# Optimization experiments

Hardware: AMD Instinct MI355X
Metric: run time of the kernel (lower is better)

The kernel has to match this reference:

```python
import jax, jax.numpy as jnp
import numpy as np

D = 256      # n_feature
LVL = 17     # tree depth (leaf levels)
MIX = 20     # M mixture components


def _lstm_cell(x, h, c, Wih, Whh, bih, bhh):
    # torch.nn.LSTMCell gate order: i, f, g, o
    g = x @ Wih.T + bih + h @ Whh.T + bhh
    i, f, gg, o = jnp.split(g, 4, axis=1)
    c2 = jax.nn.sigmoid(f) * c + jax.nn.sigmoid(i) * jnp.tanh(gg)
    return jax.nn.sigmoid(o) * jnp.tanh(c2), c2


def _get_parameter(y, M):
    parts = jnp.split(y[:, :13 * M], 13, axis=1)
    pi = jax.nn.softmax(parts[0], axis=1)
    mu_x, mu_y = parts[1], parts[2]
    sx, sy = jnp.exp(parts[3]), jnp.exp(parts[4])
    rho_xy = jnp.tanh(parts[5])
    mu_a, mu_b = parts[6], parts[7]
    sa, sb = jnp.exp(parts[8]), jnp.exp(parts[9])
    rho_ab = jnp.tanh(parts[10])
    mu_s, ss = parts[11], jnp.exp(parts[12])
    q = jax.nn.softmax(y[:, -3:], axis=1)
    return (pi, mu_x, mu_y, sx, sy, rho_xy, mu_a, mu_b, sa, sb, rho_ab, mu_s, ss, q)


def _bvn_logpdf(dx, dy, mx, my, sx, sy, rho):
    zx = (dx - mx) / sx
    zy = (dy - my) / sy
    Z = zx ** 2 + zy ** 2 - 2.0 * rho * zx * zy
    return -Z / (2.0 * (1.0 - rho ** 2)) - jnp.log(2.0 * jnp.pi * sx * sy * jnp.sqrt(1.0 - rho ** 2))


def _nll(pt, prm):
    # pt: [n, 8] = (x, y, a, b, slope, p1, p2, p3); prm: GMM parameters, each [n, M]
    pi, mx, my, sx, sy, rxy, ma, mb, sa, sb, rab, ms, ss, q = prm
    lpi = jnp.log(pi)
    dx, dy, da, db, ds = (pt[:, k:k + 1] for k in range(5))
    p = pt[:, 5:8]
    lse = jax.scipy.special.logsumexp
    lxy = lse(lpi + _bvn_logpdf(dx, dy, mx, my, sx, sy, rxy), axis=1)
    lab = lse(lpi + _bvn_logpdf(da, db, ma, mb, sa, sb, rab), axis=1)
    lsl = lse(lpi - (ds - ms) ** 2 / (2.0 * ss ** 2) - jnp.log(jnp.sqrt(2.0 * jnp.pi) * ss), axis=1)
    pen = -(p * jnp.log(q)).sum(axis=1)
    return -(lxy + lab + lsl) + pen


def _expected_pos(prm):
    pi, mx, my, sx, sy, rxy, ma, mb, sa, sb, rab, ms, ss, q = prm
    e = lambda m: (pi * m).sum(axis=1)
    return jnp.concatenate([jnp.stack([e(mx), e(my), e(ma), e(mb), e(ms)], axis=1), q], axis=1)


def _levels(I_flat):
    # I_flat is bottom-up concatenation of per-level [ni,3] blocks of a full binary tree
    n_int = I_flat.shape[0]
    L = int(np.log2(n_int + 1))
    sizes = [2 ** (L - 1 - i) for i in range(L)]
    offs = np.concatenate([[0], np.cumsum(sizes)])
    return [I_flat[offs[i]:offs[i + 1]] for i in range(L)]


def setup_inputs() -> dict:
    key = jax.random.key(0)
    ks = jax.random.split(key, 16)
    N = 2 ** (LVL + 1) - 1  # 262143 total nodes
    # heap-layout full binary tree: children of i are 2i+1, 2i+2; bottom-up levels
    blocks = []
    for l in range(LVL - 1, -1, -1):
        f = np.arange(2 ** l - 1, 2 ** (l + 1) - 1)
        blocks.append(np.stack([2 * f + 1, 2 * f + 2, f], axis=1))
    I_flat = jnp.asarray(np.concatenate(blocks, 0), dtype=jnp.int32)
    s = 0.05
    return {
        "X": jax.random.normal(ks[0], (N, 8), jnp.float32),
        "Feature": jax.random.normal(ks[1], (N, D), jnp.float32),
        "I_flat": I_flat,
        "W_ih_e": jax.random.normal(ks[2], (4 * (D // 2), 8), jnp.float32) * s,
        "W_hh_e": jax.random.normal(ks[3], (4 * (D // 2), D // 2), jnp.float32) * s,
        "b_ih_e": jax.random.normal(ks[4], (4 * (D // 2),), jnp.float32) * s,
        "b_hh_e": jax.random.normal(ks[5], (4 * (D // 2),), jnp.float32) * s,
        "fc_h_W": jax.random.normal(ks[6], (2 * D, D), jnp.float32) * s,
        "fc_h_b": jax.random.normal(ks[7], (2 * D,), jnp.float32) * s,
        "W_ih_d": jax.random.normal(ks[8], (4 * D, D + 8), jnp.float32) * s,
        "W_hh_d": jax.random.normal(ks[9], (4 * D, D), jnp.float32) * s,
        "b_ih_d": jax.random.normal(ks[10], (4 * D,), jnp.float32) * s,
        "b_hh_d": jax.random.normal(ks[11], (4 * D,), jnp.float32) * s,
        "fc_W": jax.random.normal(ks[12], (13 * MIX + 3, D // 2), jnp.float32) * s,
        "fc_b": jax.random.normal(ks[13], (13 * MIX + 3,), jnp.float32) * s,
    }


def reference(X, Feature, I_flat, W_ih_e, W_hh_e, b_ih_e, b_hh_e,
              fc_h_W, fc_h_b, W_ih_d, W_hh_d, b_ih_d, b_hh_d, fc_W, fc_b):
    levels = _levels(I_flat)
    num_I = len(levels)

    # ---- encode: bottom-up gather children -> LSTMCell -> scatter father ----
    Feature_New = Feature
    for I in levels:
        li, ri, fi = I[:, 0], I[:, 1], I[:, 2]
        hl, cl = jnp.split(Feature[li], 2, axis=1)
        hr, cr = jnp.split(Feature[ri], 2, axis=1)
        hlo, clo = _lstm_cell(X[li], hl, cl, W_ih_e, W_hh_e, b_ih_e, b_hh_e)
        hro, cro = _lstm_cell(X[ri], hr, cr, W_ih_e, W_hh_e, b_ih_e, b_hh_e)
        out = jnp.concatenate([hlo + hro, clo + cro], axis=1)
        Feature_New = Feature_New.at[fi].set(out)

    # ---- decode: top-down gather father -> LSTMCell+GMM head -> scatter children ----
    X_P = X
    Feat = Feature_New
    Loss = jnp.float32(0.0)
    for I in reversed(levels):
        li, ri, fi = I[:, 0], I[:, 1], I[:, 2]
        p_l, p_r, p_f = X[li], X[ri], X[fi]
        f_f = Feat[fi]
        z = jnp.tanh(f_f @ fc_h_W.T + fc_h_b)
        h_f, c_f = jnp.split(z, 2, axis=1)
        h_o, c_o = _lstm_cell(jnp.concatenate([p_f, f_f], axis=1), h_f, c_f,
                              W_ih_d, W_hh_d, b_ih_d, b_hh_d)
        h_left, h_right = jnp.split(h_o, 2, axis=1)
        c_left, c_right = jnp.split(c_o, 2, axis=1)
        prm_l = _get_parameter(h_left @ fc_W.T + fc_b, MIX)
        prm_r = _get_parameter(h_right @ fc_W.T + fc_b, MIX)
        direct = _nll(p_l, prm_l) + _nll(p_r, prm_r)
        swapped = _nll(p_l, prm_r) + _nll(p_r, prm_l)
        sw = swapped < direct  # l_r_index == 1 -> swap left/right outputs
        Loss = Loss + jnp.mean(jnp.where(sw, swapped, direct))
        pos_l, pos_r = _expected_pos(prm_l), _expected_pos(prm_r)
        feat_l = jnp.concatenate([h_left, c_left], axis=1)
        feat_r = jnp.concatenate([h_right, c_right], axis=1)
        swc = sw[:, None]
        Feat = Feat.at[li].set(jnp.where(swc, feat_r, feat_l))
        Feat = Feat.at[ri].set(jnp.where(swc, feat_l, feat_r))
        X_P = X_P.at[li].set(jnp.where(swc, pos_r, pos_l))
        X_P = X_P.at[ri].set(jnp.where(swc, pos_l, pos_r))
    return Loss / num_I
```

## Files before the change

### kernel.cpp

```cpp
#include <hip/hip_runtime.h>
#include <hip/hip_bf16.h>
#include <math.h>


#define LOG2PI 1.8378770664093453f

typedef __attribute__((ext_vector_type(8))) short short8;
typedef __attribute__((ext_vector_type(4))) float f32x4;

__device__ inline float frcp(float x) { return __builtin_amdgcn_rcpf(x); }
__device__ inline float fexp(float x) { return __expf(x); }
__device__ inline float flog(float x) { return __logf(x); }
__device__ inline float ftanh(float x) {
    float xc = fminf(fmaxf(x, -10.f), 10.f);
    float e = __expf(2.f * xc);
    return (e - 1.f) * frcp(e + 1.f);
}
__device__ inline float sigm(float x) {
    float xc = fminf(fmaxf(x, -30.f), 30.f);
    return frcp(1.f + __expf(-xc));
}

__device__ inline ushort f2b(float v) {
    union { float f; unsigned u; } x; x.f = v;
    unsigned r = x.u + 0x7fffu + ((x.u >> 16) & 1u);
    return (ushort)(r >> 16);
}
__device__ inline float b2f(ushort h) {
    union { unsigned u; float f; } x; x.u = ((unsigned)h) << 16; return x.f;
}

__device__ inline void gload16(const void* g, void* l) {
    __builtin_amdgcn_global_load_lds(
        (const __attribute__((address_space(1))) unsigned*)g,
        (__attribute__((address_space(3))) unsigned*)l, 16, 0, 0);
}

__device__ inline f32x4 mfma16(short8 a, short8 b, f32x4 c) {
    return __builtin_amdgcn_mfma_f32_16x16x32_bf16(a, b, c, 0, 0, 0);
}

__device__ inline float halfmax(float v) {
    #pragma unroll
    for (int o = 16; o >= 1; o >>= 1) v = fmaxf(v, __shfl_xor(v, o));
    return v;
}
__device__ inline float halfsum(float v) {
    #pragma unroll
    for (int o = 16; o >= 1; o >>= 1) v += __shfl_xor(v, o);
    return v;
}
__device__ inline float lse20(float t) {
    float m = halfmax(t);
    float s = halfsum(fexp(t - m));
    return m + flog(s);
}

__device__ inline float nll_node(const ushort* yb, const float* X,
                                 long long fi, int lane, bool& sw_out)
{
    const int half = lane >> 5, k = lane & 31;
    float v = (k < 20) ? b2f(yb[k]) : -INFINITY;
    float mm = halfmax(v);
    float se = halfsum((k < 20) ? fexp(v - mm) : 0.f);
    float lpi = v - mm - flog(se);
    float mx = 0, my = 0, rsx = 1, rsy = 1, rho = 0, hro = 0, cxy = 0;
    float ma = 0, mb2 = 0, rsa = 1, rsb = 1, rab = 0, hra = 0, cab = 0;
    float ms = 0, hrs = 0, csl = 0;
    if (k < 20) {
        mx = b2f(yb[20 + k]); my = b2f(yb[40 + k]);
        float lsx = b2f(yb[60 + k]), lsy = b2f(yb[80 + k]);
        rsx = fexp(-lsx); rsy = fexp(-lsy);
        rho = ftanh(b2f(yb[100 + k]));
        float omr = 1.f - rho * rho;
        hro = 0.5f * frcp(omr);
        cxy = LOG2PI + lsx + lsy + 0.5f * flog(omr);
        ma = b2f(yb[120 + k]); mb2 = b2f(yb[140 + k]);
        float lsa = b2f(yb[160 + k]), lsb = b2f(yb[180 + k]);
        rsa = fexp(-lsa); rsb = fexp(-lsb);
        rab = ftanh(b2f(yb[200 + k]));
        float omr2 = 1.f - rab * rab;
        hra = 0.5f * frcp(omr2);
        cab = LOG2PI + lsa + lsb + 0.5f * flog(omr2);
        ms = b2f(yb[220 + k]); float lss = b2f(yb[240 + k]);
        float rss = fexp(-lss);
        hrs = 0.5f * rss * rss;
        csl = 0.5f * LOG2PI + lss;
    }
    float lq0, lq1, lq2;
    {
        float q0 = b2f(yb[260]), q1 = b2f(yb[261]), q2 = b2f(yb[262]);
        float qm = fmaxf(q0, fmaxf(q1, q2));
        float l = flog(fexp(q0 - qm) + fexp(q1 - qm) + fexp(q2 - qm)) + qm;
        lq0 = q0 - l; lq1 = q1 - l; lq2 = q2 - l;
    }
    const float* pl = X + (size_t)(2 * fi + 1) * 8;
    const float* pr = X + (size_t)(2 * fi + 2) * 8;
    float res[2];
    #pragma unroll
    for (int s = 0; s < 2; ++s) {
        const float* pt = s ? pr : pl;
        float dx = pt[0], dy = pt[1], da = pt[2], db = pt[3], ds = pt[4];
        float t1 = -INFINITY, t2 = -INFINITY, t3 = -INFINITY;
        if (k < 20) {
            float zx = (dx - mx) * rsx, zy = (dy - my) * rsy;
            float Zz = zx * zx + zy * zy - 2.f * rho * zx * zy;
            t1 = lpi - Zz * hro - cxy;
            float za = (da - ma) * rsa, zb = (db - mb2) * rsb;
            float Z2 = za * za + zb * zb - 2.f * rab * za * zb;
            t2 = lpi - Z2 * hra - cab;
            float zs = ds - ms;
            t3 = lpi - zs * zs * hrs - csl;
        }
        float l1 = lse20(t1), l2 = lse20(t2), l3 = lse20(t3);
        float pen = -(pt[5] * lq0 + pt[6] * lq1 + pt[7] * lq2);
        res[s] = -(l1 + l2 + l3) + pen;
    }
    float Aval = half ? res[1] : res[0];
    float Bval = half ? res[0] : res[1];
    float direct = Aval + __shfl_xor(Aval, 32);
    float swapped = Bval + __shfl_xor(Bval, 32);
    sw_out = swapped < direct;
    return sw_out ? swapped : direct;
}

__device__ inline void feat_write_ap(ushort* Ap, const ushort* Hj,
                                     const ushort* Cj, long long fi, bool sw,
                                     int lane)
{
    const size_t rowL = 2 * (size_t)fi + 1;
    const int offL = sw ? 128 : 0;
    const int offR = 128 - offL;
    const int part = lane >> 5;
    const int c = (lane & 31) * 4;
    ushort4 vL = *(const ushort4*)((part ? Cj : Hj) + offL + c);
    ushort4 vR = *(const ushort4*)((part ? Cj : Hj) + offR + c);
    *(ushort4*)(Ap + rowL * 576 + 8 + part * 128 + c) = vL;
    *(ushort4*)(Ap + (rowL + 1) * 576 + 8 + part * 128 + c) = vR;
}

__global__ __launch_bounds__(256) void z_gemm(
    ushort* __restrict__ Apc,
    const ushort* __restrict__ Wz,
    const float* __restrict__ fc_h_b,
    ushort* __restrict__ Zcc,
    int M)
{
    __shared__ ushort As[128 * 64];
    __shared__ ushort Bs[128 * 64];
    const int tid = threadIdx.x;
    const int lane = tid & 63;
    const int w = tid >> 6;
    const int wr = w >> 1, wc = w & 1;
    const int fr = lane & 15, fq = lane >> 4;
    const int m0 = blockIdx.x * 128, n0 = blockIdx.y * 128;

    f32x4 acc[4][4] = {};

    #pragma unroll
    for (int k0 = 0; k0 < 256; k0 += 64) {
        __syncthreads();
        #pragma unroll
        for (int it = 0; it < 4; ++it) {
            const int i = it * 256 + tid;
            const int row = i >> 3, slot = i & 7;
            const int sl = slot ^ (row & 7);
            const int wbase = (i - lane) * 8;
            {
                int gm = m0 + row; gm = gm < M ? gm : M - 1;
                gload16(Apc + (size_t)gm * 576 + 8 + k0 + sl * 8, &As[wbase]);
            }
            {
                int gn = n0 + row; gn = gn < 512 ? gn : 511;
                gload16(Wz + (size_t)gn * 256 + k0 + sl * 8, &Bs[wbase]);
            }
        }
        __syncthreads();
        #pragma unroll
        for (int ks = 0; ks < 2; ++ks) {
            short8 af[4], bfr[4];
            #pragma unroll
            for (int mr = 0; mr < 4; ++mr) {
                const int row = wr * 64 + mr * 16 + fr;
                const int sl = (ks * 4 + fq) ^ (row & 7);
                af[mr] = *(const short8*)&As[row * 64 + sl * 8];
            }
            #pragma unroll
            for (int nc = 0; nc < 4; ++nc) {
                const int row = wc * 64 + nc * 16 + fr;
                const int sl = (ks * 4 + fq) ^ (row & 7);
                bfr[nc] = *(const short8*)&Bs[row * 64 + sl * 8];
            }
            #pragma unroll
            for (int mr = 0; mr < 4; ++mr)
                #pragma unroll
                for (int nc = 0; nc < 4; ++nc)
                    acc[mr][nc] = mfma16(af[mr], bfr[nc], acc[mr][nc]);
        }
    }

    #pragma unroll
    for (int mr = 0; mr < 4; ++mr) {
        #pragma unroll
        for (int j = 0; j < 4; ++j) {
            const int row = m0 + wr * 64 + mr * 16 + fq * 4 + j;
            if (row >= M) continue;
            #pragma unroll
            for (int nc = 0; nc < 4; ++nc) {
                const int col = n0 + wc * 64 + nc * 16 + fr;
                const float z = ftanh(acc[mr][nc][j] + fc_h_b[col]);
                if (col < 256)
                    Apc[(size_t)row * 576 + 264 + col] = f2b(z);
                else
                    Zcc[(size_t)row * 256 + (col - 256)] = f2b(z);
            }
        }
    }
}

__global__ __launch_bounds__(256) void gates_lstm(
    const ushort* __restrict__ Apc,
    const ushort* __restrict__ Wg,
    const float*  __restrict__ bg,
    const ushort* __restrict__ Zcc,
    ushort* __restrict__ H, ushort* __restrict__ C, int M)
{
    __shared__ ushort As[128 * 64];
    __shared__ ushort Bs[128 * 64];
    const int tid = threadIdx.x;
    const int lane = tid & 63;
    const int w = tid >> 6;
    const int wr = w >> 1, wc = w & 1;
    const int fr = lane & 15, fq = lane >> 4;
    const int m0 = blockIdx.x * 128, n0 = blockIdx.y * 128;

    f32x4 acc[4][4] = {};

    #pragma unroll
    for (int k0 = 0; k0 < 576; k0 += 64) {
        __syncthreads();
        #pragma unroll
        for (int it = 0; it < 4; ++it) {
            const int i = it * 256 + tid;
            const int row = i >> 3, slot = i & 7;
            const int sl = slot ^ (row & 7);
            const int wbase = (i - lane) * 8;
            {
                int gm = m0 + row; gm = gm < M ? gm : M - 1;
                gload16(Apc + (size_t)gm * 576 + k0 + sl * 8, &As[wbase]);
            }
            gload16(Wg + (size_t)(n0 + row) * 576 + k0 + sl * 8, &Bs[wbase]);
        }
        __syncthreads();
        #pragma unroll
        for (int ks = 0; ks < 2; ++ks) {
            short8 af[4], bfr[4];
            #pragma unroll
            for (int mr = 0; mr < 4; ++mr) {
                const int row = wr * 64 + mr * 16 + fr;
                const int sl = (ks * 4 + fq) ^ (row & 7);
                af[mr] = *(const short8*)&As[row * 64 + sl * 8];
            }
            #pragma unroll
            for (int nc = 0; nc < 4; ++nc) {
                const int row = wc * 64 + nc * 16 + fr;
                const int sl = (ks * 4 + fq) ^ (row & 7);
                bfr[nc] = *(const short8*)&Bs[row * 64 + sl * 8];
            }
            #pragma unroll
            for (int mr = 0; mr < 4; ++mr)
                #pragma unroll
                for (int nc = 0; nc < 4; ++nc)
                    acc[mr][nc] = mfma16(af[mr], bfr[nc], acc[mr][nc]);
        }
    }

    const int q = fr & 3;
    #pragma unroll
    for (int mr = 0; mr < 4; ++mr) {
        const int node = m0 + wr * 64 + mr * 16 + fq * 4 + q;
        #pragma unroll
        for (int nc = 0; nc < 4; ++nc) {
            const int col = n0 + wc * 64 + nc * 16 + fr;
            f32x4 v = acc[mr][nc];
            const float b = bg[col];
            v[0] += b; v[1] += b; v[2] += b; v[3] += b;
            float gv[4];
            gv[q] = v[q];
            #pragma unroll
            for (int m = 1; m < 4; ++m)
                gv[q ^ m] = __shfl_xor(v[q ^ m], m);
            if (node < M) {
                const int t = (col >> 2) & 255;
                const float cf = b2f(Zcc[(size_t)node * 256 + t]);
                const float c2 = sigm(gv[1]) * cf + sigm(gv[0]) * ftanh(gv[2]);
                const float hv = sigm(gv[3]) * ftanh(c2);
                H[(size_t)node * 256 + t] = f2b(hv);
                C[(size_t)node * 256 + t] = f2b(c2);
            }
        }
    }
}

#define YS 272
__global__ __launch_bounds__(256) void ynll(
    const ushort* __restrict__ Hb, const ushort* __restrict__ Cc,
    const ushort* __restrict__ Wyp,
    const float* __restrict__ fc_b, const float* __restrict__ X,
    ushort* __restrict__ Ap, float* __restrict__ loss,
    int Bc, long long nb_fi, float scale, int writeFeat)
{
    __shared__ char pool[17408] __attribute__((aligned(16)));
    __shared__ float lsum[4];
    ushort* Hs  = (ushort*)pool;
    ushort* Ysb = (ushort*)pool;
    const int tid = threadIdx.x;
    const int lane = tid & 63;
    const int wv = tid >> 6;
    const int fr = lane & 15, fq = lane >> 4;
    const int n16 = blockIdx.x * 16;

    #pragma unroll
    for (int it = 0; it < 2; ++it) {
        const int i = it * 256 + tid;
        const int row = i >> 4, slot = i & 15;
        const int sl = slot ^ (row & 7);
        int gr = n16 * 2 + row;
        const int grmax = 2 * Bc - 1;
        gr = gr <= grmax ? gr : grmax;
        gload16(Hb + (size_t)gr * 128 + sl * 8, &Hs[(i - lane) * 8]);
    }
    __syncthreads();

    f32x4 acc[2][5] = {};
    #pragma unroll
    for (int ks = 0; ks < 4; ++ks) {
        short8 a[2];
        #pragma unroll
        for (int rf = 0; rf < 2; ++rf) {
            const int row = rf * 16 + fr;
            const int sl = (ks * 4 + fq) ^ (row & 7);
            a[rf] = *(const short8*)&Hs[row * 128 + sl * 8];
        }
        #pragma unroll
        for (int n = 0; n < 5; ++n) {
            const short8 b = *(const short8*)(
                Wyp + (size_t)(wv * 80 + n * 16 + fr) * 128 + ks * 32 + fq * 8);
            acc[0][n] = mfma16(a[0], b, acc[0][n]);
            acc[1][n] = mfma16(a[1], b, acc[1][n]);
        }
    }
    __syncthreads();

    #pragma unroll
    for (int rf = 0; rf < 2; ++rf)
        #pragma unroll
        for (int n = 0; n < 5; ++n)
            #pragma unroll
            for (int j = 0; j < 4; ++j) {
                const int row = rf * 16 + fq * 4 + j;
                const int col = wv * 80 + n * 16 + fr;
                if (col < 263)
                    Ysb[row * YS + col] = f2b(acc[rf][n][j] + fc_b[col]);
            }
    __syncthreads();

    float wsum = 0.f;
    #pragma unroll
    for (int s4 = 0; s4 < 4; ++s4) {
        const int jj = wv * 4 + s4;
        const int j = n16 + jj;
        if (j >= Bc) break;
        bool sw;
        const long long fi = nb_fi + j;
        wsum += nll_node(&Ysb[(2 * jj + (lane >> 5)) * YS], X, fi, lane, sw);
        if (writeFeat)
            feat_write_ap(Ap, Hb + (size_t)j * 256, Cc + (size_t)j * 256,
                          fi, sw, lane);
    }
    if (lane == 0) lsum[wv] = wsum;
    __syncthreads();
    if (tid == 0)
        atomicAdd(loss, (lsum[0] + lsum[1] + lsum[2] + lsum[3]) * scale);
}

__global__ __launch_bounds__(256) void pack_all(
    const float* __restrict__ fc_h_W, ushort* __restrict__ Wz,
    const float* __restrict__ Wih, const float* __restrict__ Whh,
    ushort* __restrict__ Wg,
    const float* __restrict__ bih, const float* __restrict__ bhh,
    float* __restrict__ bg,
    const float* __restrict__ fcW, ushort* __restrict__ Wy,
    const float* __restrict__ X, ushort* __restrict__ Ap, int nInt)
{
    int i = blockIdx.x * 256 + threadIdx.x;
    if (i < 131072) { Wz[i] = f2b(fc_h_W[i]); return; }
    i -= 131072;
    if (i < 589824) {
        int np = i / 576, c = i - np * 576;
        int n = (np & 3) * 256 + (np >> 2);
        float v = 0.f;
        if (c < 264) v = Wih[n * 264 + c];
        else if (c < 520) v = Whh[n * 256 + (c - 264)];
        Wg[i] = f2b(v);
        return;
    }
    i -= 589824;
    if (i < 1024) {
        int n = (i & 3) * 256 + (i >> 2);
        bg[i] = bih[n] + bhh[n];
        return;
    }
    i -= 1024;
    if (i < 40960) {
        int r = i / 128;
        Wy[i] = f2b(r < 263 ? fcW[i] : 0.f);
        return;
    }
    i -= 40960;
    if (i < nInt * 8) {
        int row = i >> 3, s = i & 7;
        if (s == 0) {
            const float* xs = X + (size_t)row * 8;
            short8 v;
            #pragma unroll
            for (int k = 0; k < 8; ++k)
                ((ushort*)&v)[k] = f2b(xs[k]);
            *(short8*)(Ap + (size_t)row * 576) = v;
        } else {
            short8 z = {0, 0, 0, 0, 0, 0, 0, 0};
            *(short8*)(Ap + (size_t)row * 576 + (64 + s) * 8) = z;
        }
    }
}

__global__ __launch_bounds__(256) void encoder_root(
    const float* __restrict__ X, const float* __restrict__ Feature,
    const float* __restrict__ Wih, const float* __restrict__ Whh,
    const float* __restrict__ bih, const float* __restrict__ bhh,
    ushort* __restrict__ Ap)
{
    __shared__ float gsh[2][512];
    __shared__ float hc[2][256];
    const int t = threadIdx.x;
    for (int ch = 0; ch < 2; ++ch) {
        const int node = 1 + ch;
        const float* x = X + node * 8;
        const float* h = Feature + (size_t)node * 256;
        #pragma unroll
        for (int gi = 0; gi < 2; ++gi) {
            int g = t + gi * 256;
            float s = bih[g] + bhh[g];
            const float* wi = Wih + (size_t)g * 8;
            #pragma unroll
            for (int k = 0; k < 8; ++k) s += wi[k] * x[k];
            const float* wh = Whh + (size_t)g * 128;
            for (int k = 0; k < 128; ++k) s += wh[k] * h[k];
            gsh[ch][g] = s;
        }
    }
    __syncthreads();
    {
        int ch = t >> 7, u = t & 127;
        float i_ = gsh[ch][u], f_ = gsh[ch][128 + u];
        float gg = gsh[ch][256 + u], o_ = gsh[ch][384 + u];
        float c = Feature[(size_t)(1 + ch) * 256 + 128 + u];
        float c2 = sigm(f_) * c + sigm(i_) * ftanh(gg);
        hc[ch][u] = sigm(o_) * ftanh(c2);
        hc[ch][128 + u] = c2;
    }
    __syncthreads();
    Ap[8 + t] = f2b(hc[0][t] + hc[1][t]);
}

extern "C" void kernel_launch(void* const* d_in, const int* in_sizes, int n_in,
                              void* d_out, int out_size, void* d_ws, size_t ws_size,
                              hipStream_t stream)
{
    const float* X       = (const float*)d_in[0];
    const float* Feature = (const float*)d_in[1];
    const float* W_ih_e  = (const float*)d_in[3];
    const float* W_hh_e  = (const float*)d_in[4];
    const float* b_ih_e  = (const float*)d_in[5];
    const float* b_hh_e  = (const float*)d_in[6];
    const float* fc_h_W  = (const float*)d_in[7];
    const float* fc_h_b  = (const float*)d_in[8];
    const float* W_ih_d  = (const float*)d_in[9];
    const float* W_hh_d  = (const float*)d_in[10];
    const float* b_ih_d  = (const float*)d_in[11];
    const float* b_hh_d  = (const float*)d_in[12];
    const float* fc_W    = (const float*)d_in[13];
    const float* fc_b    = (const float*)d_in[14];
    const int Nnodes = in_sizes[0] / 8;
    const int nInt = (Nnodes - 1) / 2;

    float* out = (float*)d_out;
    hipMemsetAsync(d_out, 0, sizeof(float), stream);

    char* cur = (char*)d_ws;
    auto take = [&](size_t bytes) {
        char* p = cur;
        cur += (bytes + 255) & ~(size_t)255;
        return p;
    };
    ushort* Ap  = (ushort*)take((size_t)(nInt + 1) * 576 * 2);
    ushort* Wz  = (ushort*)take((size_t)512 * 256 * 2);
    ushort* Wg  = (ushort*)take((size_t)1024 * 576 * 2);
    ushort* Wy  = (ushort*)take((size_t)320 * 128 * 2);
    float*  bg  = (float*) take((size_t)1024 * 4);
    ushort* Zcc = (ushort*)take((size_t)65536 * 256 * 2);
    ushort* Hb  = (ushort*)take((size_t)65536 * 256 * 2);
    ushort* Cc  = (ushort*)take((size_t)65536 * 256 * 2);

    const int packTotal = 131072 + 589824 + 1024 + 40960 + nInt * 8;
    pack_all<<<(packTotal + 255) / 256, 256, 0, stream>>>(
        fc_h_W, Wz, W_ih_d, W_hh_d, Wg, b_ih_d, b_hh_d, bg, fc_W, Wy,
        X, Ap, nInt);

    encoder_root<<<1, 256, 0, stream>>>(X, Feature, W_ih_e, W_hh_e,
                                        b_ih_e, b_hh_e, Ap);

    for (int l = 0; l < 17; ++l) {
        const int B = 1 << l;
        const long long nb = B - 1;
        const int writeFeat = (l < 16) ? 1 : 0;
        const float scale = 1.f / ((float)B * 17.f);
        const int mg = (B + 127) / 128;
        ushort* Apc = Ap + (size_t)nb * 576;
        z_gemm<<<dim3(mg, 4), 256, 0, stream>>>(Apc, Wz, fc_h_b, Zcc, B);
        gates_lstm<<<dim3(mg, 8), 256, 0, stream>>>(
            Apc, Wg, bg, Zcc, Hb, Cc, B);
        ynll<<<(B + 15) / 16, 256, 0, stream>>>(
            Hb, Cc, Wy, fc_b, X, Ap, out,
            B, nb, scale, writeFeat);
    }
}
```

Baseline: 1.231 ms.

## Fuse z-GEMM, gate LSTM and NLL into one kernel for small levels

Adds a level_fused kernel that runs the fc_h projection, the decoder LSTM gate GEMM with cell update, and the output projection with NLL and feature write-back in a single launch. Each block handles 32 nodes and keeps intermediates in shared memory. It is used for tree levels 0-10, which cuts three launches per level to one for the launch-bound small levels. The cost is reduced parallelism, with few blocks streaming the full weight matrices from global memory for each tile, plus extra syncs within the block.

New measurement: 1.776 ms. +44.3%, slower.

```diff
diff --git a/kernel.cpp b/kernel.cpp
--- a/kernel.cpp
+++ b/kernel.cpp
@@ -139,6 +139,191 @@
     *(ushort4*)(Ap + (rowL + 1) * 576 + 8 + part * 128 + c) = vR;
 }
 
+__global__ __launch_bounds__(256) void level_fused(
+    const float* __restrict__ X, ushort* __restrict__ Ap,
+    const ushort* __restrict__ Wz, const float* __restrict__ fc_h_b,
+    const ushort* __restrict__ Wg, const float* __restrict__ bg,
+    const ushort* __restrict__ Wyp, const float* __restrict__ fc_b,
+    ushort* __restrict__ Hb, ushort* __restrict__ Cc,
+    float* __restrict__ loss, int B, long long nb, float scale)
+{
+    __shared__ char pool[53248] __attribute__((aligned(16)));
+    __shared__ float lsum[4];
+    ushort* Asm = (ushort*)pool;
+    ushort* Zc  = (ushort*)(pool + 36864);
+    ushort* Hs  = (ushort*)pool;
+    ushort* Ysb = (ushort*)pool;
+
+    const int tid = threadIdx.x;
+    const int lane = tid & 63;
+    const int wv  = tid >> 6;
+    const int fr = lane & 15, fq = lane >> 4;
+    const int gbase = blockIdx.x * 32;
+
+    for (int c = tid; c < 1280; c += 256) {
+        const int r = c / 40, s5 = c - r * 40;
+        const int s = s5 < 33 ? s5 : s5 + 32;
+        const int ss = s ^ (r & 7);
+        short8 v = {0, 0, 0, 0, 0, 0, 0, 0};
+        if (s < 33) {
+            int node = gbase + r; node = node < B ? node : B - 1;
+            v = *(const short8*)(Ap + (size_t)(nb + node) * 576 + s * 8);
+        }
+        *(short8*)&Asm[r * 576 + ss * 8] = v;
+    }
+    __syncthreads();
+
+    {
+        f32x4 acc[2][8] = {};
+        for (int ks = 0; ks < 8; ++ks) {
+            short8 a[2];
+            #pragma unroll
+            for (int mf = 0; mf < 2; ++mf) {
+                const int r = mf * 16 + fr;
+                const int ss = (1 + ks * 4 + fq) ^ (r & 7);
+                a[mf] = *(const short8*)&Asm[r * 576 + ss * 8];
+            }
+            #pragma unroll
+            for (int nf = 0; nf < 8; ++nf) {
+                const short8 b = *(const short8*)(
+                    Wz + (size_t)(wv * 128 + nf * 16 + fr) * 256 + ks * 32 + fq * 8);
+                acc[0][nf] = mfma16(a[0], b, acc[0][nf]);
+                acc[1][nf] = mfma16(a[1], b, acc[1][nf]);
+            }
+        }
+        #pragma unroll
+        for (int mf = 0; mf < 2; ++mf)
+            #pragma unroll
+            for (int nf = 0; nf < 8; ++nf)
+                #pragma unroll
+                for (int j = 0; j < 4; ++j) {
+                    const int r = mf * 16 + fq * 4 + j;
+                    const int col = wv * 128 + nf * 16 + fr;
+                    const float z = ftanh(acc[mf][nf][j] + fc_h_b[col]);
+                    if (col < 256) {
+                        const int ss = (33 + (col >> 3)) ^ (r & 7);
+                        Asm[r * 576 + ss * 8 + (col & 7)] = f2b(z);
+                    } else {
+                        Zc[r * 256 + (col - 256)] = f2b(z);
+                    }
+                }
+    }
+    __syncthreads();
+
+    for (int p = 0; p < 2; ++p) {
+        f32x4 acc[2][8] = {};
+        const int cbase = wv * 256 + p * 128;
+        for (int ks = 0; ks < 18; ++ks) {
+            short8 a[2];
+            #pragma unroll
+            for (int mf = 0; mf < 2; ++mf) {
+                const int r = mf * 16 + fr;
+                const int ss = (ks * 4 + fq) ^ (r & 7);
+                a[mf] = *(const short8*)&Asm[r * 576 + ss * 8];
+            }
+            #pragma unroll
+            for (int nf = 0; nf < 8; ++nf) {
+                const short8 b = *(const short8*)(
+                    Wg + (size_t)(cbase + nf * 16 + fr) * 576 + ks * 32 + fq * 8);
+                acc[0][nf] = mfma16(a[0], b, acc[0][nf]);
+                acc[1][nf] = mfma16(a[1], b, acc[1][nf]);
+            }
+        }
+        const int q = fr & 3;
+        #pragma unroll
+        for (int mf = 0; mf < 2; ++mf) {
+            const int r = mf * 16 + fq * 4 + q;
+            #pragma unroll
+            for (int nf = 0; nf < 8; ++nf) {
+                const int col = cbase + nf * 16 + fr;
+                f32x4 v = acc[mf][nf];
+                const float bb = bg[col];
+                v[0] += bb; v[1] += bb; v[2] += bb; v[3] += bb;
+                float gv[4];
+                gv[q] = v[q];
+                #pragma unroll
+                for (int m = 1; m < 4; ++m)
+                    gv[q ^ m] = __shfl_xor(v[q ^ m], m);
+                const int jl = gbase + r;
+                if (jl < B) {
+                    const int t = col >> 2;
+                    const float cf = b2f(Zc[r * 256 + t]);
+                    const float c2 = sigm(gv[1]) * cf + sigm(gv[0]) * ftanh(gv[2]);
+                    const float hv = sigm(gv[3]) * ftanh(c2);
+                    Hb[(size_t)jl * 256 + t] = f2b(hv);
+                    Cc[(size_t)jl * 256 + t] = f2b(c2);
+                }
+            }
+        }
+    }
+    __syncthreads();
+
+    for (int sub = 0; sub < 2; ++sub) {
+        const int n16 = gbase + sub * 16;
+        if (n16 < B) {
+            #pragma unroll
+            for (int it = 0; it < 2; ++it) {
+                const int i = it * 256 + tid;
+                const int row = i >> 4, slot = i & 15;
+                const int sl = slot ^ (row & 7);
+                int gr = n16 * 2 + row;
+                const int grmax = 2 * B - 1;
+                gr = gr <= grmax ? gr : grmax;
+                gload16(Hb + (size_t)gr * 128 + sl * 8, &Hs[(i - lane) * 8]);
+            }
+            __syncthreads();
+            f32x4 acc[2][5] = {};
+            #pragma unroll
+            for (int ks = 0; ks < 4; ++ks) {
+                short8 a[2];
+                #pragma unroll
+                for (int rf = 0; rf < 2; ++rf) {
+                    const int row = rf * 16 + fr;
+                    const int sl = (ks * 4 + fq) ^ (row & 7);
+                    a[rf] = *(const short8*)&Hs[row * 128 + sl * 8];
+                }
+                #pragma unroll
+                for (int n = 0; n < 5; ++n) {
+                    const short8 b = *(const short8*)(
+                        Wyp + (size_t)(wv * 80 + n * 16 + fr) * 128 + ks * 32 + fq * 8);
+                    acc[0][n] = mfma16(a[0], b, acc[0][n]);
+                    acc[1][n] = mfma16(a[1], b, acc[1][n]);
+                }
+            }
+            __syncthreads();
+            #pragma unroll
+            for (int rf = 0; rf < 2; ++rf)
+                #pragma unroll
+                for (int n = 0; n < 5; ++n)
+                    #pragma unroll
+                    for (int j = 0; j < 4; ++j) {
+                        const int row = rf * 16 + fq * 4 + j;
+                        const int col = wv * 80 + n * 16 + fr;
+                        if (col < 263)
+                            Ysb[row * 272 + col] = f2b(acc[rf][n][j] + fc_b[col]);
+                    }
+            __syncthreads();
+            float wsum = 0.f;
+            #pragma unroll
+            for (int s4 = 0; s4 < 4; ++s4) {
+                const int jj = wv * 4 + s4;
+                const int j = n16 + jj;
+                if (j >= B) break;
+                bool sw;
+                const long long fi = nb + j;
+                wsum += nll_node(&Ysb[(2 * jj + (lane >> 5)) * 272], X, fi, lane, sw);
+                feat_write_ap(Ap, Hb + (size_t)j * 256, Cc + (size_t)j * 256,
+                              fi, sw, lane);
+            }
+            if (lane == 0) lsum[wv] = wsum;
+            __syncthreads();
+            if (tid == 0)
+                atomicAdd(loss, (lsum[0] + lsum[1] + lsum[2] + lsum[3]) * scale);
+            __syncthreads();
+        }
+    }
+}
+
 __global__ __launch_bounds__(256) void z_gemm(
     ushort* __restrict__ Apc,
     const ushort* __restrict__ Wz,
@@ -520,7 +705,15 @@
     encoder_root<<<1, 256, 0, stream>>>(X, Feature, W_ih_e, W_hh_e,
                                         b_ih_e, b_hh_e, Ap);
 
-    for (int l = 0; l < 17; ++l) {
+    for (int l = 0; l <= 10; ++l) {
+        const int B = 1 << l;
+        const long long nb = B - 1;
+        const float scale = 1.f / ((float)B * 17.f);
+        level_fused<<<(B + 31) / 32, 256, 0, stream>>>(
+            X, Ap, Wz, fc_h_b, Wg, bg, Wy, fc_b, Hb, Cc, out, B, nb, scale);
+    }
+
+    for (int l = 11; l < 17; ++l) {
         const int B = 1 << l;
         const long long nb = B - 1;
         const int writeFeat = (l < 16) ? 1 : 0;
```
